# Kernel optimization log

Hardware: AMD Instinct MI355X
Metric: run time of the kernel (lower is better)

Reference implementation:

```python
import jax, jax.numpy as jnp
from jax import lax
import numpy as np

WIN = 9
PAD = WIN // 2  # 4 -> SAME output size
SIM_FACTOR = 1.0
REG_FACTOR = 0.1
EPS = 1e-5

_DN = ('NCHW', 'OIHW', 'NCHW')


def box_sum(x):
    """9x9 sliding-window sum via two separable 1D ones-convs (same math as a 9x9 ones conv2d)."""
    kh = jnp.ones((1, 1, WIN, 1), x.dtype)
    kw = jnp.ones((1, 1, 1, WIN), x.dtype)
    y = lax.conv_general_dilated(x, kh, (1, 1), [(PAD, PAD), (0, 0)], dimension_numbers=_DN)
    return lax.conv_general_dilated(y, kw, (1, 1), [(0, 0), (PAD, PAD)], dimension_numbers=_DN)


def ncc2d(Ii, Ji):
    win_size = float(WIN * WIN)
    I_sum = box_sum(Ii)
    J_sum = box_sum(Ji)
    I2_sum = box_sum(Ii * Ii)
    J2_sum = box_sum(Ji * Ji)
    IJ_sum = box_sum(Ii * Ji)
    u_I = I_sum / win_size
    u_J = J_sum / win_size
    cross = IJ_sum - u_J * I_sum - u_I * J_sum + u_I * u_J * win_size
    I_var = I2_sum - 2.0 * u_I * I_sum + u_I * u_I * win_size
    J_var = J2_sum - 2.0 * u_J * J_sum + u_J * u_J * win_size
    cc = cross * cross / (I_var * J_var + EPS)
    return -jnp.mean(cc)


def grad2d_l2(y_pred):
    dy = y_pred[:, :, 1:, :] - y_pred[:, :, :-1, :]
    dx = y_pred[:, :, :, 1:] - y_pred[:, :, :, :-1]
    return (jnp.mean(dx * dx) + jnp.mean(dy * dy)) / 2.0


def setup_inputs() -> dict:
    key = jax.random.key(0)
    k1, k2, k3 = jax.random.split(key, 3)
    B, H, W = 64, 512, 512
    return {
        'target_proj': jax.random.uniform(k1, (B, 1, H, W), dtype=jnp.float32),
        'warped_moving': jax.random.uniform(k2, (B, 1, H, W), dtype=jnp.float32),
        'phi': jax.random.normal(k3, (B, 2, H, W), dtype=jnp.float32),
    }


def reference(target_proj, warped_moving, phi):
    loss_sim = ncc2d(target_proj, warped_moving) * SIM_FACTOR
    loss_reg = grad2d_l2(phi) * REG_FACTOR
    total = loss_sim + loss_reg
    return (loss_sim, loss_reg, total)
```

## Files before the change

### kernel.cpp

```cpp
#include <hip/hip_runtime.h>

#define HH 512
#define WW 512
#define RSTRIP 16
#define PWC 520

__global__ __launch_bounds__(256) void ncc_kernel(const float* __restrict__ I,
                                                  const float* __restrict__ J,
                                                  float* __restrict__ ws) {
    __shared__ float vs[2][5][PWC];
    const int T = threadIdx.x;
    const int c0 = T << 1;
    const int b = blockIdx.x >> 5;
    const int r0 = (blockIdx.x & 31) << 4;

    const float* Ib = I + (size_t)b * (HH * WW);
    const float* Jb = J + (size_t)b * (HH * WW);

    if (T < 80) {
        const int buf = T / 40, rem = T % 40, p = rem >> 3, k = rem & 7;
        vs[buf][p][(k < 4) ? k : (512 + k)] = 0.f;
    }

    float2 hi[11], hj[11];
#pragma unroll
    for (int s = 0; s < 11; ++s) {
        const int r = r0 + s - 4;
        if (r >= 0) {
            hi[s] = *reinterpret_cast<const float2*>(Ib + (size_t)r * WW + c0);
            hj[s] = *reinterpret_cast<const float2*>(Jb + (size_t)r * WW + c0);
        } else {
            hi[s] = make_float2(0.f, 0.f);
            hj[s] = make_float2(0.f, 0.f);
        }
    }

    float VS[5][2] = {{0.f, 0.f}};
#pragma unroll
    for (int s = 0; s <= 8; ++s) {
        const float i0 = hi[s].x, i1 = hi[s].y;
        const float j0 = hj[s].x, j1 = hj[s].y;
        VS[0][0] += i0;                 VS[0][1] += i1;
        VS[1][0] += j0;                 VS[1][1] += j1;
        VS[2][0] = fmaf(i0, i0, VS[2][0]); VS[2][1] = fmaf(i1, i1, VS[2][1]);
        VS[3][0] = fmaf(j0, j0, VS[3][0]); VS[3][1] = fmaf(j1, j1, VS[3][1]);
        VS[4][0] = fmaf(i0, j0, VS[4][0]); VS[4][1] = fmaf(i1, j1, VS[4][1]);
    }

    const float inv81 = 1.f / 81.f;
    float acc = 0.f;

#pragma unroll
    for (int h = 0; h < RSTRIP; ++h) {
#pragma unroll
        for (int p = 0; p < 5; ++p)
            *reinterpret_cast<float2*>(&vs[h & 1][p][4 + c0]) =
                make_float2(VS[p][0], VS[p][1]);

        const int rp = (r0 + h + 7 > HH - 1) ? HH - 1 : (r0 + h + 7);
        float2 nLi = *reinterpret_cast<const float2*>(Ib + (size_t)rp * WW + c0);
        float2 nLj = *reinterpret_cast<const float2*>(Jb + (size_t)rp * WW + c0);

        __syncthreads();

        float box[5][2];
#pragma unroll
        for (int p = 0; p < 5; ++p) {
            const float2* q = reinterpret_cast<const float2*>(&vs[h & 1][p][0]) + T;
            float2 a = q[0], bb = q[1], c = q[2], d = q[3], e = q[4];
            float s = (((a.x + a.y) + (bb.x + bb.y)) +
                       ((c.x + c.y) + (d.x + d.y))) + e.x;
            box[p][0] = s;
            box[p][1] = s + (e.y - a.x);
        }
#pragma unroll
        for (int o = 0; o < 2; ++o) {
            const float IS = box[0][o], JS = box[1][o];
            const float I2 = box[2][o], J2 = box[3][o], IJ = box[4][o];
            const float cross = fmaf(-(IS * JS), inv81, IJ);
            const float Iv = fmaf(-(IS * IS), inv81, I2);
            const float Jv = fmaf(-(JS * JS), inv81, J2);
            acc = fmaf(cross * cross,
                       __builtin_amdgcn_rcpf(fmaf(Iv, Jv, 1e-5f)), acc);
        }

        if (r0 + h + 5 < HH) {
            const float2 li = hi[(h + 9) % 11], lj = hj[(h + 9) % 11];
            VS[0][0] += li.x;                 VS[0][1] += li.y;
            VS[1][0] += lj.x;                 VS[1][1] += lj.y;
            VS[2][0] = fmaf(li.x, li.x, VS[2][0]); VS[2][1] = fmaf(li.y, li.y, VS[2][1]);
            VS[3][0] = fmaf(lj.x, lj.x, VS[3][0]); VS[3][1] = fmaf(lj.y, lj.y, VS[3][1]);
            VS[4][0] = fmaf(li.x, lj.x, VS[4][0]); VS[4][1] = fmaf(li.y, lj.y, VS[4][1]);
        }
        {
            const float2 ti = hi[h % 11], tj = hj[h % 11];
            VS[0][0] -= ti.x;                 VS[0][1] -= ti.y;
            VS[1][0] -= tj.x;                 VS[1][1] -= tj.y;
            VS[2][0] = fmaf(-ti.x, ti.x, VS[2][0]); VS[2][1] = fmaf(-ti.y, ti.y, VS[2][1]);
            VS[3][0] = fmaf(-tj.x, tj.x, VS[3][0]); VS[3][1] = fmaf(-tj.y, tj.y, VS[3][1]);
            VS[4][0] = fmaf(-ti.x, tj.x, VS[4][0]); VS[4][1] = fmaf(-ti.y, tj.y, VS[4][1]);
        }
        hi[h % 11] = nLi;
        hj[h % 11] = nLj;
    }

#pragma unroll
    for (int off = 32; off; off >>= 1) acc += __shfl_down(acc, off);
    __syncthreads();
    if ((T & 63) == 0) vs[0][0][T >> 6] = acc;
    __syncthreads();
    if (T == 0)
        atomicAdd(&ws[0], (vs[0][0][0] + vs[0][0][1]) +
                          (vs[0][0][2] + vs[0][0][3]));
}

__global__ __launch_bounds__(256) void reg_kernel(const float* __restrict__ P,
                                                  float* __restrict__ ws) {
    __shared__ float sh[8];
    const int T = threadIdx.x;
    const int c4 = T & 127;
    const int strip = (blockIdx.x << 1) | (T >> 7);
    const size_t row0 = (size_t)strip << 5;
    const bool slast = ((strip & 15) == 15);
    const float* rp = P + row0 * WW + (c4 << 2);

    float sdx = 0.f, sdy = 0.f;
    float4 cur = *reinterpret_cast<const float4*>(rp);
#pragma unroll 8
    for (int i = 0; i < 32; ++i) {
        float d0 = cur.y - cur.x, d1 = cur.z - cur.y, d2 = cur.w - cur.z;
        sdx += d0 * d0 + d1 * d1 + d2 * d2;
        if (c4 < 127) {
            float nx = rp[(size_t)i * WW + 4];
            float d3 = nx - cur.w;
            sdx += d3 * d3;
        }
        if (i < 31) {
            float4 nr = *reinterpret_cast<const float4*>(rp + (size_t)(i + 1) * WW);
            float e0 = nr.x - cur.x, e1 = nr.y - cur.y;
            float e2 = nr.z - cur.z, e3 = nr.w - cur.w;
            sdy += e0 * e0 + e1 * e1 + e2 * e2 + e3 * e3;
            cur = nr;
        } else if (!slast) {
            float4 nr = *reinterpret_cast<const float4*>(rp + (size_t)32 * WW);
            float e0 = nr.x - cur.x, e1 = nr.y - cur.y;
            float e2 = nr.z - cur.z, e3 = nr.w - cur.w;
            sdy += e0 * e0 + e1 * e1 + e2 * e2 + e3 * e3;
        }
    }

#pragma unroll
    for (int off = 32; off; off >>= 1) {
        sdx += __shfl_down(sdx, off);
        sdy += __shfl_down(sdy, off);
    }
    if ((T & 63) == 0) { sh[T >> 6] = sdx; sh[4 + (T >> 6)] = sdy; }
    __syncthreads();
    if (T == 0) {
        atomicAdd(&ws[1], sh[0] + sh[1] + sh[2] + sh[3]);
        atomicAdd(&ws[2], sh[4] + sh[5] + sh[6] + sh[7]);
    }
}

__global__ void finalize_kernel(const float* __restrict__ ws,
                                float* __restrict__ out) {
    float cc_sum = ws[0], dx_sum = ws[1], dy_sum = ws[2];
    float loss_sim = -(cc_sum / 16777216.f);
    float mdx = dx_sum / 33488896.f;
    float mdy = dy_sum / 33488896.f;
    float loss_reg = (mdx + mdy) * 0.5f * 0.1f;
    out[0] = loss_sim;
    out[1] = loss_reg;
    out[2] = loss_sim + loss_reg;
}

extern "C" void kernel_launch(void* const* d_in, const int* in_sizes, int n_in,
                              void* d_out, int out_size, void* d_ws, size_t ws_size,
                              hipStream_t stream) {
    const float* I = (const float*)d_in[0];
    const float* J = (const float*)d_in[1];
    const float* P = (const float*)d_in[2];
    float* out = (float*)d_out;
    float* ws = (float*)d_ws;

    hipMemsetAsync(d_ws, 0, 3 * sizeof(float), stream);
    ncc_kernel<<<2048, 256, 0, stream>>>(I, J, ws);
    reg_kernel<<<1024, 256, 0, stream>>>(P, ws);
    finalize_kernel<<<1, 1, 0, stream>>>(ws, out);
}
```

Measured before the change: 103.1 us.

## Use single-wave blocks with 8 columns per lane and drop block barriers

Result: slower. 215.5 us (+109.0%).

```diff
diff --git a/kernel.cpp b/kernel.cpp
--- a/kernel.cpp
+++ b/kernel.cpp
@@ -2,49 +2,65 @@
 
 #define HH 512
 #define WW 512
-#define RSTRIP 16
+#define RSTRIP 8
 #define PWC 520
 
-__global__ __launch_bounds__(256) void ncc_kernel(const float* __restrict__ I,
-                                                  const float* __restrict__ J,
-                                                  float* __restrict__ ws) {
-    __shared__ float vs[2][5][PWC];
-    const int T = threadIdx.x;
-    const int c0 = T << 1;
-    const int b = blockIdx.x >> 5;
-    const int r0 = (blockIdx.x & 31) << 4;
+__global__ __launch_bounds__(64) void ncc_kernel(const float* __restrict__ I,
+                                                 const float* __restrict__ J,
+                                                 float* __restrict__ ws) {
+    __shared__ float vsrow[5][PWC];
+    const int L = threadIdx.x;
+    const int c0 = L << 3;
+    const int b = blockIdx.x >> 6;
+    const int r0 = (blockIdx.x & 63) << 3;
 
     const float* Ib = I + (size_t)b * (HH * WW);
     const float* Jb = J + (size_t)b * (HH * WW);
 
-    if (T < 80) {
-        const int buf = T / 40, rem = T % 40, p = rem >> 3, k = rem & 7;
-        vs[buf][p][(k < 4) ? k : (512 + k)] = 0.f;
-    }
-
-    float2 hi[11], hj[11];
-#pragma unroll
-    for (int s = 0; s < 11; ++s) {
-        const int r = r0 + s - 4;
+    if (L < 40) {
+        const int p = L >> 3, k = L & 7;
+        vsrow[p][(k < 4) ? k : (512 + k)] = 0.f;
+    }
+
+    float VS[5][8];
+#pragma unroll
+    for (int p = 0; p < 5; ++p)
+#pragma unroll
+        for (int c = 0; c < 8; ++c) VS[p][c] = 0.f;
+
+#pragma unroll
+    for (int s = 0; s < 9; ++s) {
+        const int r = r0 - 4 + s;
         if (r >= 0) {
-            hi[s] = *reinterpret_cast<const float2*>(Ib + (size_t)r * WW + c0);
-            hj[s] = *reinterpret_cast<const float2*>(Jb + (size_t)r * WW + c0);
-        } else {
-            hi[s] = make_float2(0.f, 0.f);
-            hj[s] = make_float2(0.f, 0.f);
-        }
-    }
-
-    float VS[5][2] = {{0.f, 0.f}};
-#pragma unroll
-    for (int s = 0; s <= 8; ++s) {
-        const float i0 = hi[s].x, i1 = hi[s].y;
-        const float j0 = hj[s].x, j1 = hj[s].y;
-        VS[0][0] += i0;                 VS[0][1] += i1;
-        VS[1][0] += j0;                 VS[1][1] += j1;
-        VS[2][0] = fmaf(i0, i0, VS[2][0]); VS[2][1] = fmaf(i1, i1, VS[2][1]);
-        VS[3][0] = fmaf(j0, j0, VS[3][0]); VS[3][1] = fmaf(j1, j1, VS[3][1]);
-        VS[4][0] = fmaf(i0, j0, VS[4][0]); VS[4][1] = fmaf(i1, j1, VS[4][1]);
+            const float4* ip = reinterpret_cast<const float4*>(Ib + (size_t)r * WW + c0);
+            const float4* jp = reinterpret_cast<const float4*>(Jb + (size_t)r * WW + c0);
+            const float4 i4a = ip[0], i4b = ip[1], j4a = jp[0], j4b = jp[1];
+            const float iv[8] = {i4a.x, i4a.y, i4a.z, i4a.w, i4b.x, i4b.y, i4b.z, i4b.w};
+            const float jv[8] = {j4a.x, j4a.y, j4a.z, j4a.w, j4b.x, j4b.y, j4b.z, j4b.w};
+#pragma unroll
+            for (int c = 0; c < 8; ++c) {
+                VS[0][c] += iv[c];
+                VS[1][c] += jv[c];
+                VS[2][c] = fmaf(iv[c], iv[c], VS[2][c]);
+                VS[3][c] = fmaf(jv[c], jv[c], VS[3][c]);
+                VS[4][c] = fmaf(iv[c], jv[c], VS[4][c]);
+            }
+        }
+    }
+
+    float4 pLi[2][2], pLj[2][2], pTi[2][2], pTj[2][2];
+    {
+        const int jt1 = (r0 - 4 < 0) ? 0 : r0 - 4;
+        const int jt2 = (r0 - 3 < 0) ? 0 : r0 - 3;
+        const float4* p;
+        p = reinterpret_cast<const float4*>(Ib + (size_t)(r0 + 5) * WW + c0); pLi[1][0] = p[0]; pLi[1][1] = p[1];
+        p = reinterpret_cast<const float4*>(Jb + (size_t)(r0 + 5) * WW + c0); pLj[1][0] = p[0]; pLj[1][1] = p[1];
+        p = reinterpret_cast<const float4*>(Ib + (size_t)jt1 * WW + c0);      pTi[1][0] = p[0]; pTi[1][1] = p[1];
+        p = reinterpret_cast<const float4*>(Jb + (size_t)jt1 * WW + c0);      pTj[1][0] = p[0]; pTj[1][1] = p[1];
+        p = reinterpret_cast<const float4*>(Ib + (size_t)(r0 + 6) * WW + c0); pLi[0][0] = p[0]; pLi[0][1] = p[1];
+        p = reinterpret_cast<const float4*>(Jb + (size_t)(r0 + 6) * WW + c0); pLj[0][0] = p[0]; pLj[0][1] = p[1];
+        p = reinterpret_cast<const float4*>(Ib + (size_t)jt2 * WW + c0);      pTi[0][0] = p[0]; pTi[0][1] = p[1];
+        p = reinterpret_cast<const float4*>(Jb + (size_t)jt2 * WW + c0);      pTj[0][0] = p[0]; pTj[0][1] = p[1];
     }
 
     const float inv81 = 1.f / 81.f;
@@ -52,29 +68,73 @@
 
 #pragma unroll
     for (int h = 0; h < RSTRIP; ++h) {
-#pragma unroll
-        for (int p = 0; p < 5; ++p)
-            *reinterpret_cast<float2*>(&vs[h & 1][p][4 + c0]) =
-                make_float2(VS[p][0], VS[p][1]);
-
-        const int rp = (r0 + h + 7 > HH - 1) ? HH - 1 : (r0 + h + 7);
-        float2 nLi = *reinterpret_cast<const float2*>(Ib + (size_t)rp * WW + c0);
-        float2 nLj = *reinterpret_cast<const float2*>(Jb + (size_t)rp * WW + c0);
-
-        __syncthreads();
-
-        float box[5][2];
+        if (h >= 1) {
+            const int bk = h & 1;
+            if (r0 + h + 4 < HH) {
+                const float lv[8] = {pLi[bk][0].x, pLi[bk][0].y, pLi[bk][0].z, pLi[bk][0].w,
+                                     pLi[bk][1].x, pLi[bk][1].y, pLi[bk][1].z, pLi[bk][1].w};
+                const float mv[8] = {pLj[bk][0].x, pLj[bk][0].y, pLj[bk][0].z, pLj[bk][0].w,
+                                     pLj[bk][1].x, pLj[bk][1].y, pLj[bk][1].z, pLj[bk][1].w};
+#pragma unroll
+                for (int c = 0; c < 8; ++c) {
+                    VS[0][c] += lv[c];
+                    VS[1][c] += mv[c];
+                    VS[2][c] = fmaf(lv[c], lv[c], VS[2][c]);
+                    VS[3][c] = fmaf(mv[c], mv[c], VS[3][c]);
+                    VS[4][c] = fmaf(lv[c], mv[c], VS[4][c]);
+                }
+            }
+            if (r0 + h - 5 >= 0) {
+                const float tv[8] = {pTi[bk][0].x, pTi[bk][0].y, pTi[bk][0].z, pTi[bk][0].w,
+                                     pTi[bk][1].x, pTi[bk][1].y, pTi[bk][1].z, pTi[bk][1].w};
+                const float uv[8] = {pTj[bk][0].x, pTj[bk][0].y, pTj[bk][0].z, pTj[bk][0].w,
+                                     pTj[bk][1].x, pTj[bk][1].y, pTj[bk][1].z, pTj[bk][1].w};
+#pragma unroll
+                for (int c = 0; c < 8; ++c) {
+                    VS[0][c] -= tv[c];
+                    VS[1][c] -= uv[c];
+                    VS[2][c] = fmaf(-tv[c], tv[c], VS[2][c]);
+                    VS[3][c] = fmaf(-uv[c], uv[c], VS[3][c]);
+                    VS[4][c] = fmaf(-tv[c], uv[c], VS[4][c]);
+                }
+            }
+            if (h + 2 <= RSTRIP - 1) {
+                const int jl = (r0 + h + 6 > HH - 1) ? HH - 1 : r0 + h + 6;
+                const int jt = (r0 + h - 3 < 0) ? 0 : r0 + h - 3;
+                const float4* p;
+                p = reinterpret_cast<const float4*>(Ib + (size_t)jl * WW + c0); pLi[bk][0] = p[0]; pLi[bk][1] = p[1];
+                p = reinterpret_cast<const float4*>(Jb + (size_t)jl * WW + c0); pLj[bk][0] = p[0]; pLj[bk][1] = p[1];
+                p = reinterpret_cast<const float4*>(Ib + (size_t)jt * WW + c0); pTi[bk][0] = p[0]; pTi[bk][1] = p[1];
+                p = reinterpret_cast<const float4*>(Jb + (size_t)jt * WW + c0); pTj[bk][0] = p[0]; pTj[bk][1] = p[1];
+            }
+        }
+
 #pragma unroll
         for (int p = 0; p < 5; ++p) {
-            const float2* q = reinterpret_cast<const float2*>(&vs[h & 1][p][0]) + T;
-            float2 a = q[0], bb = q[1], c = q[2], d = q[3], e = q[4];
-            float s = (((a.x + a.y) + (bb.x + bb.y)) +
-                       ((c.x + c.y) + (d.x + d.y))) + e.x;
+            *reinterpret_cast<float4*>(&vsrow[p][4 + c0]) =
+                make_float4(VS[p][0], VS[p][1], VS[p][2], VS[p][3]);
+            *reinterpret_cast<float4*>(&vsrow[p][8 + c0]) =
+                make_float4(VS[p][4], VS[p][5], VS[p][6], VS[p][7]);
+        }
+
+        float box[5][8];
+#pragma unroll
+        for (int p = 0; p < 5; ++p) {
+            const float4* q = reinterpret_cast<const float4*>(&vsrow[p][c0]);
+            const float4 w0 = q[0], w1 = q[1], w2 = q[2], w3 = q[3];
+            const float w[16] = {w0.x, w0.y, w0.z, w0.w, w1.x, w1.y, w1.z, w1.w,
+                                 w2.x, w2.y, w2.z, w2.w, w3.x, w3.y, w3.z, w3.w};
+            float s = (((w[0] + w[1]) + (w[2] + w[3])) +
+                       ((w[4] + w[5]) + (w[6] + w[7]))) + w[8];
             box[p][0] = s;
-            box[p][1] = s + (e.y - a.x);
-        }
-#pragma unroll
-        for (int o = 0; o < 2; ++o) {
+#pragma unroll
+            for (int o = 1; o < 8; ++o) {
+                s += w[o + 8] - w[o - 1];
+                box[p][o] = s;
+            }
+        }
+#pragma unroll
+        for (int o = 0; o < 8; ++o) {
             const float IS = box[0][o], JS = box[1][o];
             const float I2 = box[2][o], J2 = box[3][o], IJ = box[4][o];
             const float cross = fmaf(-(IS * JS), inv81, IJ);
@@ -83,35 +143,11 @@
             acc = fmaf(cross * cross,
                        __builtin_amdgcn_rcpf(fmaf(Iv, Jv, 1e-5f)), acc);
         }
-
-        if (r0 + h + 5 < HH) {
-            const float2 li = hi[(h + 9) % 11], lj = hj[(h + 9) % 11];
-            VS[0][0] += li.x;                 VS[0][1] += li.y;
-            VS[1][0] += lj.x;                 VS[1][1] += lj.y;
-            VS[2][0] = fmaf(li.x, li.x, VS[2][0]); VS[2][1] = fmaf(li.y, li.y, VS[2][1]);
-            VS[3][0] = fmaf(lj.x, lj.x, VS[3][0]); VS[3][1] = fmaf(lj.y, lj.y, VS[3][1]);
-            VS[4][0] = fmaf(li.x, lj.x, VS[4][0]); VS[4][1] = fmaf(li.y, lj.y, VS[4][1]);
-        }
-        {
-            const float2 ti = hi[h % 11], tj = hj[h % 11];
-            VS[0][0] -= ti.x;                 VS[0][1] -= ti.y;
-            VS[1][0] -= tj.x;                 VS[1][1] -= tj.y;
-            VS[2][0] = fmaf(-ti.x, ti.x, VS[2][0]); VS[2][1] = fmaf(-ti.y, ti.y, VS[2][1]);
-            VS[3][0] = fmaf(-tj.x, tj.x, VS[3][0]); VS[3][1] = fmaf(-tj.y, tj.y, VS[3][1]);
-            VS[4][0] = fmaf(-ti.x, tj.x, VS[4][0]); VS[4][1] = fmaf(-ti.y, tj.y, VS[4][1]);
-        }
-        hi[h % 11] = nLi;
-        hj[h % 11] = nLj;
     }
 
 #pragma unroll
     for (int off = 32; off; off >>= 1) acc += __shfl_down(acc, off);
-    __syncthreads();
-    if ((T & 63) == 0) vs[0][0][T >> 6] = acc;
-    __syncthreads();
-    if (T == 0)
-        atomicAdd(&ws[0], (vs[0][0][0] + vs[0][0][1]) +
-                          (vs[0][0][2] + vs[0][0][3]));
+    if (L == 0) atomicAdd(&ws[0], acc);
 }
 
 __global__ __launch_bounds__(256) void reg_kernel(const float* __restrict__ P,
@@ -184,7 +220,7 @@
     float* ws = (float*)d_ws;
 
     hipMemsetAsync(d_ws, 0, 3 * sizeof(float), stream);
-    ncc_kernel<<<2048, 256, 0, stream>>>(I, J, ws);
+    ncc_kernel<<<4096, 64, 0, stream>>>(I, J, ws);
     reg_kernel<<<1024, 256, 0, stream>>>(P, ws);
     finalize_kernel<<<1, 1, 0, stream>>>(ws, out);
 }
```
